# Kernel tuning notes

Measured on AMD Instinct MI355X. Metric: run time of the kernel, lower is better.

Reference implementation:

```python
import jax, jax.numpy as jnp
import numpy as np

HEAD_SIZE = 128  # embeddings_dims // no_of_heads = 4096 // 32


def apply_rope(v):
    # v: [B, S, d] with d = HEAD_SIZE; interleaved-pair rotation as in source
    B, S, d = v.shape
    pos = jnp.arange(S, dtype=jnp.float32)[:, None]              # [S, 1]
    idx = jnp.arange(0, d, 2, dtype=jnp.float32)[None, :]        # [1, d//2]
    theta = jnp.power(10000.0, -2.0 * idx / d)                   # [1, d//2]
    angles = pos * theta                                         # [S, d//2]
    cos = jnp.cos(angles)
    sin = jnp.sin(angles)
    vr = v.reshape(B, S, d // 2, 2)
    x0, x1 = vr[..., 0], vr[..., 1]
    out = jnp.stack([x0 * cos - x1 * sin, x1 * cos + x0 * sin], axis=-1)
    return out.reshape(B, S, d)


def setup_inputs() -> dict:
    key = jax.random.key(0)
    kx, kq, kk, kv = jax.random.split(key, 4)
    B, S, D = 2, 4096, 4096
    d = HEAD_SIZE
    scale = 1.0 / np.sqrt(D)
    return {
        "x": jax.random.normal(kx, (B, S, D), dtype=jnp.float32),
        "Wq": jax.random.normal(kq, (d, D), dtype=jnp.float32) * scale,
        "Wk": jax.random.normal(kk, (d, D), dtype=jnp.float32) * scale,
        "Wv": jax.random.normal(kv, (d, D), dtype=jnp.float32) * scale,
    }


def reference(x, Wq, Wk, Wv):
    # single attention head, non-flash path (eval mode: dropout = identity)
    B, S, D = x.shape
    q = jnp.einsum('bsd,hd->bsh', x, Wq)  # [B, S, head]
    k = jnp.einsum('bsd,hd->bsh', x, Wk)
    v = jnp.einsum('bsd,hd->bsh', x, Wv)
    q = apply_rope(q)
    k = apply_rope(k)
    scale = k.shape[-1] ** (-0.5)
    scores = jnp.einsum('bqh,bkh->bqk', q, k) * scale  # [B, S, S]
    causal = jnp.tril(jnp.ones((S, S), dtype=bool))
    scores = jnp.where(causal, scores, -jnp.inf)
    weights = jax.nn.softmax(scores, axis=-1)
    out = jnp.einsum('bqk,bkh->bqh', weights, v)  # [B, S, head]
    return out
```

## Files before the change

kernel.cpp:

```cpp
#include <hip/hip_runtime.h>

typedef _Float16 half8 __attribute__((ext_vector_type(8)));
typedef _Float16 half2v __attribute__((ext_vector_type(2)));
typedef float f32x4 __attribute__((ext_vector_type(4)));

#define S_LEN 4096
#define D_DIM 4096
#define HD 128


#define QSTR 136
template<int KSPLIT>
__global__ __launch_bounds__(256) void proj_kernel(const float* __restrict__ x,
                                                   const float* __restrict__ wq,
                                                   const float* __restrict__ wk,
                                                   const float* __restrict__ wv,
                                                   _Float16* __restrict__ qw,
                                                   _Float16* __restrict__ kw,
                                                   _Float16* __restrict__ vt,
                                                   float* __restrict__ P) {
    __shared__ __align__(16) _Float16 smem[17408];
    const int tid = threadIdx.x;
    const int wg = blockIdx.x;
    const int nwg = 384 * KSPLIT;
    const int swz = (wg & 7) * (nwg >> 3) + (wg >> 3);
    const int bx = swz % 3;
    const int rest = swz / 3;
    const int ks = (KSPLIT == 2) ? (rest & 1) : 0;
    const int M0 = ((KSPLIT == 2) ? (rest >> 1) : rest) * 64;
    const int NS = 128 / KSPLIT;
    const float* w = (bx == 0) ? wq : (bx == 1) ? wk : wv;
    const int lane = tid & 63, wv_ = tid >> 6;
    const int l15 = lane & 15, quad = lane >> 4;

    const int arow = tid >> 2, acol = (tid & 3) * 8;
    const int brow = tid >> 1, bcol = (tid & 1) * 16;
    const float* xa = x + (size_t)(M0 + arow) * D_DIM + acol + ks * (D_DIM / 2);
    const float* wb = w + (size_t)brow * D_DIM + bcol + ks * (D_DIM / 2);

    const int awoff = ((arow >> 4) * 64 + (arow & 15) + (tid & 3) * 16) * 8;
    const int bwoff = ((brow >> 5) * 128 + ((brow >> 4) & 1) * 64 + (brow & 15) +
                       (tid & 1) * 32) * 8;
    const int rdoff = lane * 8;

    f32x4 acc[4][2];
    for (int mi = 0; mi < 4; ++mi)
        for (int ni = 0; ni < 2; ++ni)
            acc[mi][ni] = (f32x4){0.f, 0.f, 0.f, 0.f};

    auto stage = [&](_Float16* buf, float4 A0, float4 A1,
                     float4 B0, float4 B1, float4 B2, float4 B3) {
        half8 ha = { (_Float16)A0.x, (_Float16)A0.y, (_Float16)A0.z, (_Float16)A0.w,
                     (_Float16)A1.x, (_Float16)A1.y, (_Float16)A1.z, (_Float16)A1.w };
        half8 hb0 = { (_Float16)B0.x, (_Float16)B0.y, (_Float16)B0.z, (_Float16)B0.w,
                      (_Float16)B1.x, (_Float16)B1.y, (_Float16)B1.z, (_Float16)B1.w };
        half8 hb1 = { (_Float16)B2.x, (_Float16)B2.y, (_Float16)B2.z, (_Float16)B2.w,
                      (_Float16)B3.x, (_Float16)B3.y, (_Float16)B3.z, (_Float16)B3.w };
        *(half8*)&buf[awoff] = ha;
        *(half8*)&buf[2048 + bwoff] = hb0;
        *(half8*)&buf[2048 + bwoff + 128] = hb1;
    };
    auto compute = [&](const _Float16* buf) {
        const _Float16* Af = buf + rdoff;
        const _Float16* Bf = buf + 2048 + wv_ * 1024 + rdoff;
        half8 af[4], bf[2];
        for (int mi = 0; mi < 4; ++mi)
            af[mi] = *(const half8*)(Af + mi * 512);
        for (int ni = 0; ni < 2; ++ni)
            bf[ni] = *(const half8*)(Bf + ni * 512);
        for (int mi = 0; mi < 4; ++mi)
            for (int ni = 0; ni < 2; ++ni)
                acc[mi][ni] = __builtin_amdgcn_mfma_f32_16x16x32_f16(af[mi], bf[ni],
                                                                     acc[mi][ni], 0, 0, 0);
    };

#define LOADSET(Aa, Ab, Ba, Bb, Bc, Bd, off)                                  \
    Aa = *(const float4*)(xa + (off));     Ab = *(const float4*)(xa + (off) + 4);  \
    Ba = *(const float4*)(wb + (off));     Bb = *(const float4*)(wb + (off) + 4);  \
    Bc = *(const float4*)(wb + (off) + 8); Bd = *(const float4*)(wb + (off) + 12);

    float4 a0_0, a0_1, b0_0, b0_1, b0_2, b0_3;
    float4 a1_0, a1_1, b1_0, b1_1, b1_2, b1_3;
    LOADSET(a0_0, a0_1, b0_0, b0_1, b0_2, b0_3, 0)
    LOADSET(a1_0, a1_1, b1_0, b1_1, b1_2, b1_3, 32)

    for (int i = 0; i < NS; i += 2) {
        stage(smem, a0_0, a0_1, b0_0, b0_1, b0_2, b0_3);
        if (i + 2 < NS) {
            const int off = (i + 2) * 32;
            LOADSET(a0_0, a0_1, b0_0, b0_1, b0_2, b0_3, off)
        }
        __syncthreads();
        compute(smem);
        stage(smem + 6144, a1_0, a1_1, b1_0, b1_1, b1_2, b1_3);
        if (i + 3 < NS) {
            const int off = (i + 3) * 32;
            LOADSET(a1_0, a1_1, b1_0, b1_1, b1_2, b1_3, off)
        }
        __syncthreads();
        compute(smem + 6144);
    }
#undef LOADSET
    __syncthreads();

    if (KSPLIT == 2) {
        float* sf = (float*)smem;
        for (int mi = 0; mi < 4; ++mi)
            for (int ni = 0; ni < 2; ++ni)
                for (int r = 0; r < 4; ++r)
                    sf[(mi * 16 + quad * 4 + r) * 132 + wv_ * 32 + ni * 16 + l15] =
                        acc[mi][ni][r];
        __syncthreads();
        const int row = tid >> 2, c0 = (tid & 3) * 32;
        float* dst = P + ((size_t)(ks * 3 + bx) * 8192 + M0 + row) * HD + c0;
        for (int j = 0; j < 8; ++j)
            *(float4*)(dst + j * 4) = *(const float4*)&sf[row * 132 + c0 + j * 4];
    } else if (bx < 2) {
        for (int mi = 0; mi < 4; ++mi)
            for (int ni = 0; ni < 2; ++ni)
                for (int r = 0; r < 4; ++r)
                    smem[(mi * 16 + quad * 4 + r) * QSTR + wv_ * 32 + ni * 16 + l15] =
                        (_Float16)acc[mi][ni][r];
        __syncthreads();
        _Float16* dst = ((bx == 0) ? qw : kw) + (size_t)M0 * HD;
        const int row = tid >> 2, c0 = (tid & 3) * 32;
        for (int j = 0; j < 4; ++j)
            *(half8*)&dst[row * HD + c0 + j * 8] = *(const half8*)&smem[row * QSTR + c0 + j * 8];
    } else {
        for (int mi = 0; mi < 4; ++mi)
            for (int ni = 0; ni < 2; ++ni)
                for (int r = 0; r < 4; ++r)
                    smem[(wv_ * 32 + ni * 16 + l15) * QSTR + mi * 16 + quad * 4 + r] =
                        (_Float16)acc[mi][ni][r];
        __syncthreads();
        _Float16* dst = vt + (size_t)(M0 >> 12) * HD * S_LEN + (M0 & (S_LEN - 1));
        const int hd = tid >> 1, s0 = (tid & 1) * 32;
        for (int j = 0; j < 4; ++j)
            *(half8*)&dst[(size_t)hd * S_LEN + s0 + j * 8] =
                *(const half8*)&smem[hd * QSTR + s0 + j * 8];
    }
}

__global__ __launch_bounds__(256) void combine_kernel(const float* __restrict__ P,
                                                      _Float16* __restrict__ qw,
                                                      _Float16* __restrict__ kw,
                                                      _Float16* __restrict__ vt) {
    const int tid = threadIdx.x;
    const int M0 = blockIdx.x * 64;
    const int row = tid >> 2, c0 = (tid & 3) * 32;
    if (blockIdx.y == 0) {
        const float* Pq0 = P + ((size_t)0 * 8192 + M0 + row) * HD + c0;
        const float* Pq1 = P + ((size_t)3 * 8192 + M0 + row) * HD + c0;
        const float* Pk0 = P + ((size_t)1 * 8192 + M0 + row) * HD + c0;
        const float* Pk1 = P + ((size_t)4 * 8192 + M0 + row) * HD + c0;
        float qv[32], kv[32];
#pragma unroll
        for (int j = 0; j < 8; ++j) {
            float4 a = *(const float4*)(Pq0 + j * 4);
            float4 b = *(const float4*)(Pq1 + j * 4);
            float4 c = *(const float4*)(Pk0 + j * 4);
            float4 d = *(const float4*)(Pk1 + j * 4);
            qv[j * 4 + 0] = a.x + b.x; qv[j * 4 + 1] = a.y + b.y;
            qv[j * 4 + 2] = a.z + b.z; qv[j * 4 + 3] = a.w + b.w;
            kv[j * 4 + 0] = c.x + d.x; kv[j * 4 + 1] = c.y + d.y;
            kv[j * 4 + 2] = c.z + d.z; kv[j * 4 + 3] = c.w + d.w;
        }
        const int s = (M0 + row) & (S_LEN - 1);
        half8 oq[4], ok[4];
#pragma unroll
        for (int jp = 0; jp < 16; ++jp) {
            const int pi = (c0 >> 1) + jp;
            const float theta = exp2f((float)pi * -0.4152410118609203f);
            float sn, cn;
            sincosf((float)s * theta, &sn, &cn);
            const float q0 = qv[2 * jp], q1 = qv[2 * jp + 1];
            const float k0 = kv[2 * jp], k1 = kv[2 * jp + 1];
            oq[jp >> 2][(2 * jp) & 7]     = (_Float16)(q0 * cn - q1 * sn);
            oq[jp >> 2][(2 * jp + 1) & 7] = (_Float16)(q1 * cn + q0 * sn);
            ok[jp >> 2][(2 * jp) & 7]     = (_Float16)(k0 * cn - k1 * sn);
            ok[jp >> 2][(2 * jp + 1) & 7] = (_Float16)(k1 * cn + k0 * sn);
        }
        _Float16* qdst = qw + (size_t)(M0 + row) * HD + c0;
        _Float16* kdst = kw + (size_t)(M0 + row) * HD + c0;
#pragma unroll
        for (int j = 0; j < 4; ++j) {
            *(half8*)(qdst + j * 8) = oq[j];
            *(half8*)(kdst + j * 8) = ok[j];
        }
    } else {
        __shared__ __align__(16) _Float16 sh[128][72];
        const float* Pv0 = P + ((size_t)2 * 8192 + M0 + row) * HD + c0;
        const float* Pv1 = P + ((size_t)5 * 8192 + M0 + row) * HD + c0;
#pragma unroll
        for (int j = 0; j < 8; ++j) {
            float4 a = *(const float4*)(Pv0 + j * 4);
            float4 b = *(const float4*)(Pv1 + j * 4);
            sh[c0 + j * 4 + 0][row] = (_Float16)(a.x + b.x);
            sh[c0 + j * 4 + 1][row] = (_Float16)(a.y + b.y);
            sh[c0 + j * 4 + 2][row] = (_Float16)(a.z + b.z);
            sh[c0 + j * 4 + 3][row] = (_Float16)(a.w + b.w);
        }
        __syncthreads();
        const int hd = tid >> 1, s0 = (tid & 1) * 32;
        _Float16* dst = vt + (size_t)(M0 >> 12) * HD * S_LEN + (size_t)hd * S_LEN +
                        (M0 & (S_LEN - 1)) + s0;
        for (int j = 0; j < 4; ++j)
            *(half8*)(dst + j * 8) = *(const half8*)&sh[hd][s0 + j * 8];
    }
}

__global__ __launch_bounds__(256) void rope_kernel(_Float16* __restrict__ qw,
                                                   _Float16* __restrict__ kw) {
    const int g = blockIdx.x * 256 + threadIdx.x;
    const int m = g >> 6, p = g & 63;
    const int s = m & (S_LEN - 1);
    const float theta = exp2f((float)p * -0.4152410118609203f);
    float sn, cn;
    sincosf((float)s * theta, &sn, &cn);
    const size_t off = (size_t)m * HD + 2 * p;
    half2v qv = *(half2v*)&qw[off];
    half2v kv = *(half2v*)&kw[off];
    float q0 = qv[0], q1 = qv[1], k0 = kv[0], k1 = kv[1];
    half2v qo = { (_Float16)(q0 * cn - q1 * sn), (_Float16)(q1 * cn + q0 * sn) };
    half2v ko = { (_Float16)(k0 * cn - k1 * sn), (_Float16)(k1 * cn + k0 * sn) };
    *(half2v*)&qw[off] = qo;
    *(half2v*)&kw[off] = ko;
}

__device__ __forceinline__ void load_kf(const _Float16* __restrict__ kb, int kbase,
                                        int l15, int quad, half8* kf) {
    const _Float16* kr = kb + (size_t)(kbase + l15) * HD + quad * 8;
    for (int kk = 0; kk < 4; ++kk) {
        kf[kk]     = *(const half8*)(kr + kk * 32);
        kf[4 + kk] = *(const half8*)(kr + 16 * HD + kk * 32);
    }
}

template<bool MASKED>
__device__ __forceinline__ void attn_tile(int kbase, int qg, int l15, int quad,
                                          const half8* kf,
                                          const _Float16* __restrict__ vtb,
                                          const half8* bq, f32x4* acc,
                                          float& mrun, float& lrun) {
    const float csc = 0.1275174348796053f;
    half8 va[8];
    const _Float16* vr = vtb + (size_t)l15 * S_LEN + kbase + quad * 8;
    for (int c = 0; c < 8; ++c)
        va[c] = *(const half8*)(vr + (size_t)c * 16 * S_LEN);
    f32x4 st0 = (f32x4){0.f, 0.f, 0.f, 0.f};
    f32x4 st1 = (f32x4){0.f, 0.f, 0.f, 0.f};
    for (int kk = 0; kk < 4; ++kk) {
        st0 = __builtin_amdgcn_mfma_f32_16x16x32_f16(kf[kk],     bq[kk], st0, 0, 0, 0);
        st1 = __builtin_amdgcn_mfma_f32_16x16x32_f16(kf[4 + kk], bq[kk], st1, 0, 0, 0);
    }
    float p0[4], p1[4];
    float mloc = -1e30f;
    for (int r = 0; r < 4; ++r) {
        float v0 = st0[r] * csc;
        float v1 = st1[r] * csc;
        if (MASKED) {
            const int key0 = kbase + quad * 4 + r;
            if (key0 > qg)      v0 = -1e30f;
            if (key0 + 16 > qg) v1 = -1e30f;
        }
        p0[r] = v0; p1[r] = v1;
        mloc = fmaxf(mloc, fmaxf(v0, v1));
    }
    mloc = fmaxf(mloc, __shfl_xor(mloc, 16));
    mloc = fmaxf(mloc, __shfl_xor(mloc, 32));
    const float mnew = fmaxf(mrun, mloc);
    const float alpha = exp2f(mrun - mnew);
    mrun = mnew;
    float ls = 0.f;
    for (int r = 0; r < 4; ++r) {
        p0[r] = exp2f(p0[r] - mnew);
        p1[r] = exp2f(p1[r] - mnew);
        ls += p0[r] + p1[r];
    }
    ls += __shfl_xor(ls, 16);
    ls += __shfl_xor(ls, 32);
    lrun = lrun * alpha + ls;
    for (int c = 0; c < 8; ++c)
        acc[c] *= alpha;
    int ph0 = __builtin_bit_cast(int, __builtin_amdgcn_cvt_pkrtz(p0[0], p0[1]));
    int ph1 = __builtin_bit_cast(int, __builtin_amdgcn_cvt_pkrtz(p0[2], p0[3]));
    int ph2 = __builtin_bit_cast(int, __builtin_amdgcn_cvt_pkrtz(p1[0], p1[1]));
    int ph3 = __builtin_bit_cast(int, __builtin_amdgcn_cvt_pkrtz(p1[2], p1[3]));
    const int s0 = (l15 + (((quad << 1)    ) & 3) * 16) * 4;
    const int s1 = (l15 + (((quad << 1) + 1) & 3) * 16) * 4;
    int a0 = __builtin_amdgcn_ds_bpermute(s0, ph0);
    int a1 = __builtin_amdgcn_ds_bpermute(s0, ph1);
    int a2 = __builtin_amdgcn_ds_bpermute(s1, ph0);
    int a3 = __builtin_amdgcn_ds_bpermute(s1, ph1);
    int b0 = __builtin_amdgcn_ds_bpermute(s0, ph2);
    int b1 = __builtin_amdgcn_ds_bpermute(s0, ph3);
    int b2 = __builtin_amdgcn_ds_bpermute(s1, ph2);
    int b3 = __builtin_amdgcn_ds_bpermute(s1, ph3);
    const bool lo = quad < 2;
    int4 pi = { lo ? a0 : b0, lo ? a1 : b1, lo ? a2 : b2, lo ? a3 : b3 };
    half8 pf = __builtin_bit_cast(half8, pi);
    for (int c = 0; c < 8; ++c)
        acc[c] = __builtin_amdgcn_mfma_f32_16x16x32_f16(va[c], pf, acc[c], 0, 0, 0);
}

__global__ __launch_bounds__(256) void attn_kernel(const _Float16* __restrict__ q,
                                                   const _Float16* __restrict__ k,
                                                   const _Float16* __restrict__ vt,
                                                   float* __restrict__ out) {
    __shared__ __align__(16) float Osh[4][16][132];
    __shared__ float msh[4][16];
    __shared__ float lsh[4][16];
    const int tid = threadIdx.x;
    const int lane = tid & 63, wv_ = tid >> 6;
    const int l15 = lane & 15, quad = lane >> 4;
    const int bidx = blockIdx.x;
    const int b = bidx & 1;
    const int t = 255 - (bidx >> 1);
    const int qb = t * 16;
    const int qg = qb + l15;

    const _Float16* qp = q + (size_t)(b * S_LEN + qb) * HD;
    half8 bq[4];
    for (int kk = 0; kk < 4; ++kk)
        bq[kk] = *(const half8*)&qp[l15 * HD + kk * 32 + quad * 8];

    f32x4 acc[8];
    for (int c = 0; c < 8; ++c) acc[c] = (f32x4){0.f, 0.f, 0.f, 0.f};
    float mrun = -1e30f, lrun = 0.f;

    const _Float16* kb = k + (size_t)b * S_LEN * HD;
    const _Float16* vtb = vt + (size_t)b * HD * S_LEN;

    const int nfull = (qb + 1) >> 5;
    const int kend = nfull * 32;
    const bool hasm = ((nfull & 3) == wv_);
    const int kb0 = wv_ * 32;

    half8 kf[8], kf2[8];
    if (kb0 < kend)      load_kf(kb, kb0, l15, quad, kf);
    else if (hasm)       load_kf(kb, kend, l15, quad, kf);
    for (int kbase = kb0; kbase < kend; kbase += 128) {
        const int kn = kbase + 128;
        if (kn < kend)   load_kf(kb, kn, l15, quad, kf2);
        else if (hasm)   load_kf(kb, kend, l15, quad, kf2);
        attn_tile<false>(kbase, qg, l15, quad, kf, vtb, bq, acc, mrun, lrun);
        for (int j = 0; j < 8; ++j) kf[j] = kf2[j];
    }
    if (hasm)
        attn_tile<true>(kend, qg, l15, quad, kf, vtb, bq, acc, mrun, lrun);

    for (int c = 0; c < 8; ++c)
        *(f32x4*)&Osh[wv_][l15][c * 16 + quad * 4] = acc[c];
    if (quad == 0) { msh[wv_][l15] = mrun; lsh[wv_][l15] = lrun; }
    __syncthreads();

    const int qr = tid >> 4, dg = (tid & 15) * 8;
    float m0 = msh[0][qr], m1 = msh[1][qr], m2 = msh[2][qr], m3 = msh[3][qr];
    float mm = fmaxf(fmaxf(m0, m1), fmaxf(m2, m3));
    float f0 = exp2f(m0 - mm), f1 = exp2f(m1 - mm), f2 = exp2f(m2 - mm), f3 = exp2f(m3 - mm);
    float l = lsh[0][qr] * f0 + lsh[1][qr] * f1 + lsh[2][qr] * f2 + lsh[3][qr] * f3;
    f32x4 oa = (f32x4){0.f, 0.f, 0.f, 0.f}, ob = oa;
    oa += *(f32x4*)&Osh[0][qr][dg] * f0;  ob += *(f32x4*)&Osh[0][qr][dg + 4] * f0;
    oa += *(f32x4*)&Osh[1][qr][dg] * f1;  ob += *(f32x4*)&Osh[1][qr][dg + 4] * f1;
    oa += *(f32x4*)&Osh[2][qr][dg] * f2;  ob += *(f32x4*)&Osh[2][qr][dg + 4] * f2;
    oa += *(f32x4*)&Osh[3][qr][dg] * f3;  ob += *(f32x4*)&Osh[3][qr][dg + 4] * f3;
    const float inv = 1.0f / l;
    float* op = out + (size_t)(b * S_LEN + qb + qr) * HD + dg;
    *(float4*)op       = (float4){oa[0] * inv, oa[1] * inv, oa[2] * inv, oa[3] * inv};
    *(float4*)(op + 4) = (float4){ob[0] * inv, ob[1] * inv, ob[2] * inv, ob[3] * inv};
}

extern "C" void kernel_launch(void* const* d_in, const int* in_sizes, int n_in,
                              void* d_out, int out_size, void* d_ws, size_t ws_size,
                              hipStream_t stream) {
    const float* x  = (const float*)d_in[0];
    const float* Wq = (const float*)d_in[1];
    const float* Wk = (const float*)d_in[2];
    const float* Wv = (const float*)d_in[3];
    float* out = (float*)d_out;
    char* ws = (char*)d_ws;
    _Float16* qw = (_Float16*)(ws);
    _Float16* kw = (_Float16*)(ws + (2u << 20));
    _Float16* vt = (_Float16*)(ws + (4u << 20));
    float* P = (float*)(ws + (6u << 20));

    const size_t need = (size_t)(6u << 20) + (size_t)2 * 3 * 8192 * 128 * 4;
    if (ws_size >= need) {
        proj_kernel<2><<<dim3(768), dim3(256), 0, stream>>>(x, Wq, Wk, Wv, qw, kw, vt, P);
        combine_kernel<<<dim3(128, 2), dim3(256), 0, stream>>>(P, qw, kw, vt);
    } else {
        proj_kernel<1><<<dim3(384), dim3(256), 0, stream>>>(x, Wq, Wk, Wv, qw, kw, vt, P);
        rope_kernel<<<dim3(2048), dim3(256), 0, stream>>>(qw, kw);
    }
    attn_kernel<<<dim3(512), dim3(256), 0, stream>>>(qw, kw, vt, out);
}
```

Baseline: 367.2 us.

## Pre-convert weights to fp16 and stream B tiles via direct global-to-LDS loads

Adds a small kernel that converts Wq/Wk/Wv to fp16 once per call in workspace. The projection kernel then loads its B operand with global_load_lds straight into the LDS fragment layout, skipping register staging and per-iteration conversion. Global traffic for weights is halved and VGPR pressure drops. In exchange there is an extra launch plus a write/read of 3MB of fp16 weights, the sync placement in the double-buffer loop changes, and the larger workspace threshold may send more configs down the non-split path.

```diff
diff --git a/kernel.cpp b/kernel.cpp
--- a/kernel.cpp
+++ b/kernel.cpp
@@ -9,12 +9,31 @@
 #define HD 128
 
 
+__device__ __forceinline__ void gload_lds16(const _Float16* g, _Float16* l) {
+    __builtin_amdgcn_global_load_lds(
+        (const __attribute__((address_space(1))) unsigned int*)g,
+        (__attribute__((address_space(3))) unsigned int*)l, 16, 0, 0);
+}
+
+__global__ __launch_bounds__(256) void convw_kernel(const float* __restrict__ wq,
+                                                    const float* __restrict__ wk,
+                                                    const float* __restrict__ wv,
+                                                    _Float16* __restrict__ wh) {
+    const int g = blockIdx.x * 256 + threadIdx.x;
+    const int p = g >> 16;
+    const int off = (g & 65535) * 8;
+    const float* src = ((p == 0) ? wq : (p == 1) ? wk : wv) + off;
+    float4 v0 = *(const float4*)src;
+    float4 v1 = *(const float4*)(src + 4);
+    half8 h = { (_Float16)v0.x, (_Float16)v0.y, (_Float16)v0.z, (_Float16)v0.w,
+                (_Float16)v1.x, (_Float16)v1.y, (_Float16)v1.z, (_Float16)v1.w };
+    *(half8*)&wh[(size_t)p * 524288 + off] = h;
+}
+
 #define QSTR 136
 template<int KSPLIT>
 __global__ __launch_bounds__(256) void proj_kernel(const float* __restrict__ x,
-                                                   const float* __restrict__ wq,
-                                                   const float* __restrict__ wk,
-                                                   const float* __restrict__ wv,
+                                                   const _Float16* __restrict__ wh,
                                                    _Float16* __restrict__ qw,
                                                    _Float16* __restrict__ kw,
                                                    _Float16* __restrict__ vt,
@@ -29,18 +48,15 @@
     const int ks = (KSPLIT == 2) ? (rest & 1) : 0;
     const int M0 = ((KSPLIT == 2) ? (rest >> 1) : rest) * 64;
     const int NS = 128 / KSPLIT;
-    const float* w = (bx == 0) ? wq : (bx == 1) ? wk : wv;
     const int lane = tid & 63, wv_ = tid >> 6;
     const int l15 = lane & 15, quad = lane >> 4;
 
     const int arow = tid >> 2, acol = (tid & 3) * 8;
-    const int brow = tid >> 1, bcol = (tid & 1) * 16;
     const float* xa = x + (size_t)(M0 + arow) * D_DIM + acol + ks * (D_DIM / 2);
-    const float* wb = w + (size_t)brow * D_DIM + bcol + ks * (D_DIM / 2);
+    const _Float16* wsrc = wh + (size_t)bx * 128 * D_DIM + ks * (D_DIM / 2) +
+                           (size_t)(wv_ * 32 + l15) * D_DIM + quad * 8;
 
     const int awoff = ((arow >> 4) * 64 + (arow & 15) + (tid & 3) * 16) * 8;
-    const int bwoff = ((brow >> 5) * 128 + ((brow >> 4) & 1) * 64 + (brow & 15) +
-                       (tid & 1) * 32) * 8;
     const int rdoff = lane * 8;
 
     f32x4 acc[4][2];
@@ -48,17 +64,15 @@
         for (int ni = 0; ni < 2; ++ni)
             acc[mi][ni] = (f32x4){0.f, 0.f, 0.f, 0.f};
 
-    auto stage = [&](_Float16* buf, float4 A0, float4 A1,
-                     float4 B0, float4 B1, float4 B2, float4 B3) {
+    auto stageA = [&](_Float16* buf, float4 A0, float4 A1) {
         half8 ha = { (_Float16)A0.x, (_Float16)A0.y, (_Float16)A0.z, (_Float16)A0.w,
                      (_Float16)A1.x, (_Float16)A1.y, (_Float16)A1.z, (_Float16)A1.w };
-        half8 hb0 = { (_Float16)B0.x, (_Float16)B0.y, (_Float16)B0.z, (_Float16)B0.w,
-                      (_Float16)B1.x, (_Float16)B1.y, (_Float16)B1.z, (_Float16)B1.w };
-        half8 hb1 = { (_Float16)B2.x, (_Float16)B2.y, (_Float16)B2.z, (_Float16)B2.w,
-                      (_Float16)B3.x, (_Float16)B3.y, (_Float16)B3.z, (_Float16)B3.w };
         *(half8*)&buf[awoff] = ha;
-        *(half8*)&buf[2048 + bwoff] = hb0;
-        *(half8*)&buf[2048 + bwoff + 128] = hb1;
+    };
+    auto stageB = [&](_Float16* buf, int slab) {
+        const _Float16* s = wsrc + slab * 32;
+        gload_lds16(s,               &buf[2048 + wv_ * 1024]);
+        gload_lds16(s + 16 * D_DIM,  &buf[2048 + wv_ * 1024 + 512]);
     };
     auto compute = [&](const _Float16* buf) {
         const _Float16* Af = buf + rdoff;
@@ -74,33 +88,29 @@
                                                                      acc[mi][ni], 0, 0, 0);
     };
 
-#define LOADSET(Aa, Ab, Ba, Bb, Bc, Bd, off)                                  \
-    Aa = *(const float4*)(xa + (off));     Ab = *(const float4*)(xa + (off) + 4);  \
-    Ba = *(const float4*)(wb + (off));     Bb = *(const float4*)(wb + (off) + 4);  \
-    Bc = *(const float4*)(wb + (off) + 8); Bd = *(const float4*)(wb + (off) + 12);
-
-    float4 a0_0, a0_1, b0_0, b0_1, b0_2, b0_3;
-    float4 a1_0, a1_1, b1_0, b1_1, b1_2, b1_3;
-    LOADSET(a0_0, a0_1, b0_0, b0_1, b0_2, b0_3, 0)
-    LOADSET(a1_0, a1_1, b1_0, b1_1, b1_2, b1_3, 32)
+    float4 a0_0, a0_1, a1_0, a1_1;
+    a0_0 = *(const float4*)(xa);      a0_1 = *(const float4*)(xa + 4);
+    a1_0 = *(const float4*)(xa + 32); a1_1 = *(const float4*)(xa + 36);
+    stageB(smem, 0);
 
     for (int i = 0; i < NS; i += 2) {
-        stage(smem, a0_0, a0_1, b0_0, b0_1, b0_2, b0_3);
+        stageA(smem, a0_0, a0_1);
+        __syncthreads();
         if (i + 2 < NS) {
-            const int off = (i + 2) * 32;
-            LOADSET(a0_0, a0_1, b0_0, b0_1, b0_2, b0_3, off)
-        }
-        __syncthreads();
+            a0_0 = *(const float4*)(xa + (i + 2) * 32);
+            a0_1 = *(const float4*)(xa + (i + 2) * 32 + 4);
+        }
+        stageB(smem + 6144, i + 1);
         compute(smem);
-        stage(smem + 6144, a1_0, a1_1, b1_0, b1_1, b1_2, b1_3);
+        stageA(smem + 6144, a1_0, a1_1);
+        __syncthreads();
         if (i + 3 < NS) {
-            const int off = (i + 3) * 32;
-            LOADSET(a1_0, a1_1, b1_0, b1_1, b1_2, b1_3, off)
-        }
-        __syncthreads();
+            a1_0 = *(const float4*)(xa + (i + 3) * 32);
+            a1_1 = *(const float4*)(xa + (i + 3) * 32 + 4);
+        }
+        if (i + 2 < NS) stageB(smem, i + 2);
         compute(smem + 6144);
     }
-#undef LOADSET
     __syncthreads();
 
     if (KSPLIT == 2) {
@@ -382,14 +392,16 @@
     _Float16* qw = (_Float16*)(ws);
     _Float16* kw = (_Float16*)(ws + (2u << 20));
     _Float16* vt = (_Float16*)(ws + (4u << 20));
-    float* P = (float*)(ws + (6u << 20));
-
-    const size_t need = (size_t)(6u << 20) + (size_t)2 * 3 * 8192 * 128 * 4;
-    if (ws_size >= need) {
-        proj_kernel<2><<<dim3(768), dim3(256), 0, stream>>>(x, Wq, Wk, Wv, qw, kw, vt, P);
+    _Float16* wh = (_Float16*)(ws + (6u << 20));
+    float* P = (float*)(ws + (9u << 20));
+
+    const size_t need2 = (size_t)(9u << 20) + (size_t)2 * 3 * 8192 * 128 * 4;
+    convw_kernel<<<dim3(768), dim3(256), 0, stream>>>(Wq, Wk, Wv, wh);
+    if (ws_size >= need2) {
+        proj_kernel<2><<<dim3(768), dim3(256), 0, stream>>>(x, wh, qw, kw, vt, P);
         combine_kernel<<<dim3(128, 2), dim3(256), 0, stream>>>(P, qw, kw, vt);
     } else {
-        proj_kernel<1><<<dim3(384), dim3(256), 0, stream>>>(x, Wq, Wk, Wv, qw, kw, vt, P);
+        proj_kernel<1><<<dim3(384), dim3(256), 0, stream>>>(x, wh, qw, kw, vt, P);
         rope_kernel<<<dim3(2048), dim3(256), 0, stream>>>(qw, kw);
     }
     attn_kernel<<<dim3(512), dim3(256), 0, stream>>>(qw, kw, vt, out);
```

After: 343.4 us. -6.5%, faster.
